# Optimization experiments

Hardware: AMD Instinct MI355X
Metric: run time of the kernel (lower is better)

Reference implementation:

```python
import jax, jax.numpy as jnp
import numpy as np

B, H0, W0, D0 = 2, 28, 28, 28
C, NH, SR, WS = 96, 6, 4, 7
N = H0 * W0 * D0
EPS = 1e-5


def _window_partition(x, ws, H, W, D):
    # x: [B, heads, N, c] -> [B*heads*nWindows, ws^3, c]
    Bn, h, Nn, c = x.shape
    x = x.reshape(Bn * h, H // ws, ws, W // ws, ws, D // ws, ws, c)
    x = x.transpose(0, 1, 3, 5, 2, 4, 6, 7)
    return x.reshape(-1, ws * ws * ws, c)


def _window_reverse(w, ws, H, W, D, heads):
    # w: [B*heads*nWindows, ws^3, c] -> [B, N, heads*c]
    c = w.shape[-1]
    nW = (H // ws) * (W // ws) * (D // ws)
    Bh = w.shape[0] // nW
    x = w.reshape(Bh, H // ws, W // ws, D // ws, ws, ws, ws, c)
    x = x.transpose(0, 1, 4, 2, 5, 3, 6, 7).reshape(Bh, H, W, D, c)
    x = x.reshape(Bh // heads, heads, H, W, D, c).transpose(0, 2, 3, 4, 1, 5)
    return x.reshape(Bh // heads, H * W * D, heads * c)


def _ln(x, g, b):
    mu = x.mean(-1, keepdims=True)
    var = ((x - mu) ** 2).mean(-1, keepdims=True)
    return (x - mu) * jax.lax.rsqrt(var + EPS) * g + b


def _forward(x, H, W, D, lepe_lin_w, lepe_lin_b, lepe_conv_w, lepe_conv_b,
             sr_w, sr_b, norm_g, norm_b, q1_w, kv1_w, q2_w, kv2_w, proj_w, proj_b):
    Bn, Nn, Cc = x.shape
    nh2 = NH // 2
    hd = Cc // NH
    scale = hd ** -0.5
    dn = ('NCDHW', 'OIDHW', 'NCDHW')
    # LePE branch: linear -> depthwise 3x3x3 conv over the 3D volume
    t = (x @ lepe_lin_w.T + lepe_lin_b).transpose(0, 2, 1).reshape(Bn, Cc, H, W, D)
    lepe = jax.lax.conv_general_dilated(t, lepe_conv_w, (1, 1, 1), [(1, 1)] * 3,
                                        dimension_numbers=dn, feature_group_count=Cc)
    lepe = (lepe + lepe_conv_b[None, :, None, None, None]).reshape(Bn, Cc, Nn).transpose(0, 2, 1)
    # Branch 1: spatial-reduction global attention on half the heads
    q1 = (x @ q1_w.T).reshape(Bn, Nn, nh2, hd).transpose(0, 2, 1, 3)  # [B,h/2,N,hd]
    x5 = x.transpose(0, 2, 1).reshape(Bn, Cc, H, W, D)
    xs = jax.lax.conv_general_dilated(x5, sr_w, (SR, SR, SR), 'VALID', dimension_numbers=dn)
    xs = (xs + sr_b[None, :, None, None, None]).reshape(Bn, Cc, -1).transpose(0, 2, 1)  # [B,Nsr,C]
    xs = jax.nn.gelu(_ln(xs, norm_g, norm_b), approximate=False)
    kv1 = (xs @ kv1_w.T).reshape(Bn, -1, 2, nh2, hd).transpose(2, 0, 3, 1, 4)
    k1, v1 = kv1[0], kv1[1]
    attn1 = jax.nn.softmax(jnp.einsum('bhnd,bhmd->bhnm', q1, k1) * scale, axis=-1)
    x1 = jnp.einsum('bhnm,bhmd->bhnd', attn1, v1).transpose(0, 2, 1, 3).reshape(Bn, Nn, Cc // 2)
    # Branch 2: 7x7x7 windowed local attention on the other half of the heads
    q2 = (x @ q2_w.T).reshape(Bn, Nn, nh2, hd).transpose(0, 2, 1, 3)
    kv2 = (x @ kv2_w.T).reshape(Bn, Nn, 2, nh2, hd).transpose(2, 0, 3, 1, 4)
    k2, v2 = kv2[0], kv2[1]
    q2w = _window_partition(q2, WS, H, W, D)
    k2w = _window_partition(k2, WS, H, W, D)
    v2w = _window_partition(v2, WS, H, W, D)
    attn2 = jax.nn.softmax(jnp.einsum('wnd,wmd->wnm', q2w, k2w) * scale, axis=-1)
    x2 = _window_reverse(jnp.einsum('wnm,wmd->wnd', attn2, v2w), WS, H, W, D, nh2)
    # Fuse branches, add LePE, project
    return (jnp.concatenate([x1, x2], axis=-1) + lepe) @ proj_w.T + proj_b


def setup_inputs() -> dict:
    key = jax.random.key(0)
    ks = jax.random.split(key, 10)
    lin = lambda k, o, i: jax.random.normal(k, (o, i), jnp.float32) * 0.02
    return {
        'x': jax.random.normal(ks[0], (B, N, C), jnp.float32),
        'H': H0, 'W': W0, 'D': D0,
        'lepe_lin_w': lin(ks[1], C, C),
        'lepe_lin_b': jnp.zeros((C,), jnp.float32),
        'lepe_conv_w': jax.random.normal(ks[2], (C, 1, 3, 3, 3), jnp.float32) * 0.27,
        'lepe_conv_b': jnp.zeros((C,), jnp.float32),
        'sr_w': jax.random.normal(ks[3], (C, C, SR, SR, SR), jnp.float32) * 0.02,
        'sr_b': jnp.zeros((C,), jnp.float32),
        'norm_g': jnp.ones((C,), jnp.float32),
        'norm_b': jnp.zeros((C,), jnp.float32),
        'q1_w': lin(ks[4], C // 2, C),
        'kv1_w': lin(ks[5], C, C),
        'q2_w': lin(ks[6], C // 2, C),
        'kv2_w': lin(ks[7], C, C),
        'proj_w': lin(ks[8], C, C),
        'proj_b': jnp.zeros((C,), jnp.float32),
    }


def reference(x, H, W, D, lepe_lin_w, lepe_lin_b, lepe_conv_w, lepe_conv_b,
              sr_w, sr_b, norm_g, norm_b, q1_w, kv1_w, q2_w, kv2_w, proj_w, proj_b):
    return _forward(x, H, W, D, lepe_lin_w, lepe_lin_b, lepe_conv_w, lepe_conv_b,
                    sr_w, sr_b, norm_g, norm_b, q1_w, kv1_w, q2_w, kv2_w, proj_w, proj_b)
```

## Files before the change

kernel.cpp:

```cpp
#include <hip/hip_runtime.h>

#define BB 2
#define NTOK 21952
#define CC 96
#define WD 784
#define NSR 343
#define NKT 22
#define NPADK 9.f
#define NSITE 686
#define SCALE 0.25f
#define LN_EPS 1e-5f
#define WSA_N (6*16*24*64)
#define WPA_N (18*6*64)

typedef _Float16 half_t;
typedef __attribute__((ext_vector_type(2))) _Float16 h2;
typedef __attribute__((ext_vector_type(4))) _Float16 h4;
typedef __attribute__((ext_vector_type(8))) _Float16 h8;
typedef __attribute__((ext_vector_type(4))) float f32x4;
union HU { h8 v; h2 p[4]; };
union H4U { h4 v; h2 p[2]; };

__device__ __forceinline__ h2 pk2(float a, float b) {
    return __builtin_bit_cast(h2, __builtin_amdgcn_cvt_pkrtz(a, b));
}

__global__ __launch_bounds__(256) void k_wt(
    const float* __restrict__ w, h4* __restrict__ WSA, h4* __restrict__ WPA,
    const float* __restrict__ lepe_w, const float* __restrict__ q1_w,
    const float* __restrict__ q2_w, const float* __restrict__ kv2_w,
    const float* __restrict__ cw, float* __restrict__ cwT)
{
    const int id = blockIdx.x * 256 + threadIdx.x;
    if (id < WSA_N) {
        const int lane = id & 63;
        const int kt = (id >> 6) % 24;
        const int ks = ((id >> 6) / 24) % 16;
        const int ct = (id >> 6) / 384;
        const int co = ct * 16 + (lane & 15);
        const int kb = ks * 384 + kt * 16 + 4 * (lane >> 4);
        const int p = kb / 96, c = kb % 96;
        float f[4];
#pragma unroll
        for (int i = 0; i < 4; i++)
            f[i] = w[(size_t)co * 6144 + (c + i) * 64 + p];
        H4U t; t.p[0] = pk2(f[0], f[1]); t.p[1] = pk2(f[2], f[3]);
        WSA[id] = t.v;
    } else if (id < WSA_N + WPA_N) {
        const int id2 = id - WSA_N;
        const int lane = id2 & 63;
        const int kt = (id2 >> 6) % 6;
        const int ct = (id2 >> 6) / 6;
        const int co = ct * 16 + (lane & 15);
        const int k = kt * 16 + 4 * (lane >> 4);
        const float* wrow;
        if (co < 96)       wrow = lepe_w + co * 96;
        else if (co < 144) wrow = q1_w + (co - 96) * 96;
        else if (co < 192) wrow = q2_w + (co - 144) * 96;
        else               wrow = kv2_w + (co - 192) * 96;
        float4 v = *(const float4*)(wrow + k);
        H4U t; t.p[0] = pk2(v.x, v.y); t.p[1] = pk2(v.z, v.w);
        WPA[id2] = t.v;
    } else if (id < WSA_N + WPA_N + 27 * 96) {
        const int id3 = id - WSA_N - WPA_N;
        const int tap = id3 / 96, c = id3 % 96;
        cwT[tap * 96 + c] = cw[c * 27 + tap];
    }
}

__global__ __launch_bounds__(256) void k_proj(
    const float* __restrict__ x, const h4* __restrict__ WPA,
    const float* __restrict__ lepe_b, float* __restrict__ P)
{
    __shared__ h4 BX[4 * 6 * 64];
    const int blk = blockIdx.x;
    const int tid = threadIdx.x;

    for (int s = tid; s < 1536; s += 256) {
        int lane = s & 63;
        int kt = (s >> 6) % 6;
        int tt = (s >> 6) / 6;
        int tok = blk * 64 + tt * 16 + (lane & 15);
        int k0 = kt * 16 + 4 * (lane >> 4);
        float4 v = *(const float4*)(x + (size_t)tok * 96 + k0);
        H4U t; t.p[0] = pk2(v.x, v.y); t.p[1] = pk2(v.z, v.w);
        BX[s] = t.v;
    }
    __syncthreads();

    const int lane = tid & 63;
    const int wid = tid >> 6;

    h4 bx[24];
#pragma unroll
    for (int q = 0; q < 24; q++) bx[q] = BX[q * 64 + lane];

    for (int ct = wid; ct < 18; ct += 4) {
        f32x4 acc[4];
#pragma unroll
        for (int tt = 0; tt < 4; tt++) acc[tt] = (f32x4){0.f, 0.f, 0.f, 0.f};
#pragma unroll
        for (int kt = 0; kt < 6; kt++) {
            h4 wa = WPA[(ct * 6 + kt) * 64 + lane];
#pragma unroll
            for (int tt = 0; tt < 4; tt++)
                acc[tt] = __builtin_amdgcn_mfma_f32_16x16x16f16(
                    wa, bx[tt * 6 + kt], acc[tt], 0, 0, 0);
        }
        float4 b4 = make_float4(0.f, 0.f, 0.f, 0.f);
        if (ct < 6) b4 = *(const float4*)(lepe_b + ct * 16 + 4 * (lane >> 4));
#pragma unroll
        for (int tt = 0; tt < 4; tt++) {
            int tok = blk * 64 + tt * 16 + (lane & 15);
            float4 o = make_float4(acc[tt][0] + b4.x, acc[tt][1] + b4.y,
                                   acc[tt][2] + b4.z, acc[tt][3] + b4.w);
            *(float4*)(P + (size_t)tok * 288 + ct * 16 + 4 * (lane >> 4)) = o;
        }
    }
}

__global__ __launch_bounds__(384) void k_sr_a(
    const float* __restrict__ x, const h4* __restrict__ WSA,
    float* __restrict__ pa)
{
    __shared__ h4 BX[24 * 64];
    const int mb = blockIdx.x;
    const int ks = blockIdx.y;
    const int tid = threadIdx.x;
    const int lane = tid & 63;
    const int ct = tid >> 6;

    for (int s = tid; s < 24 * 64; s += 384) {
        int l = s & 63;
        int kt = s >> 6;
        int site = mb * 16 + (l & 15);
        if (site > NSITE - 1) site = NSITE - 1;
        int b = site / NSR, sloc = site % NSR;
        int si = sloc / 49, sj = (sloc / 7) % 7, sk = sloc % 7;
        int kg = ks * 384 + kt * 16 + 4 * (l >> 4);
        int p = kg / 96, c = kg % 96;
        int a = p >> 4, q = (p >> 2) & 3, r = p & 3;
        int n = (4 * si + a) * WD + (4 * sj + q) * 28 + (4 * sk + r);
        float4 v = *(const float4*)(x + ((size_t)b * NTOK + n) * 96 + c);
        H4U t; t.p[0] = pk2(v.x, v.y); t.p[1] = pk2(v.z, v.w);
        BX[s] = t.v;
    }
    __syncthreads();

    const int site_g = mb * 16 + (lane & 15);
    const h4* wb = WSA + (size_t)((ct * 16 + ks) * 24) * 64 + lane;

    f32x4 acc0 = (f32x4){0.f, 0.f, 0.f, 0.f};
    f32x4 acc1 = (f32x4){0.f, 0.f, 0.f, 0.f};
#pragma unroll
    for (int kp = 0; kp < 12; kp++) {
        h4 wa0 = wb[(2 * kp) * 64];
        h4 wa1 = wb[(2 * kp + 1) * 64];
        acc0 = __builtin_amdgcn_mfma_f32_16x16x16f16(
            wa0, BX[(2 * kp) * 64 + lane], acc0, 0, 0, 0);
        acc1 = __builtin_amdgcn_mfma_f32_16x16x16f16(
            wa1, BX[(2 * kp + 1) * 64 + lane], acc1, 0, 0, 0);
    }
    if (site_g < NSITE) {
        *(float4*)(pa + ((size_t)site_g * 16 + ks) * 96 + ct * 16
                   + 4 * (lane >> 4)) =
            make_float4(acc0[0] + acc1[0], acc0[1] + acc1[1],
                        acc0[2] + acc1[2], acc0[3] + acc1[3]);
    }
}

__global__ __launch_bounds__(96) void k_sr_b(
    const float* __restrict__ pa, const float* __restrict__ sr_b,
    const float* __restrict__ norm_g, const float* __restrict__ norm_b,
    const float* __restrict__ kv1_w, float* __restrict__ k1,
    float* __restrict__ v1)
{
    __shared__ float xs_s[96];
    __shared__ float gx[96];
    const int s_g = blockIdx.x;
    const int b = s_g / NSR, s = s_g % NSR;
    const int co = threadIdx.x;

    const float* pp = pa + (size_t)s_g * 16 * 96 + co;
    float acc = sr_b[co];
#pragma unroll
    for (int ks = 0; ks < 16; ks++) acc += pp[ks * 96];
    xs_s[co] = acc;
    __syncthreads();

    float m = 0.f, m2 = 0.f;
    for (int c = 0; c < 96; c++) { float v = xs_s[c]; m += v; m2 += v * v; }
    m *= (1.f / 96.f);
    float var = m2 * (1.f / 96.f) - m * m;
    float t = (acc - m) * rsqrtf(var + LN_EPS) * norm_g[co] + norm_b[co];
    gx[co] = 0.5f * t * (1.f + erff(t * 0.70710678118654752f));
    __syncthreads();

    const float4* w4 = (const float4*)(kv1_w + co * 96);
    const float4* g4 = (const float4*)gx;
    float a2 = 0.f;
#pragma unroll
    for (int c = 0; c < 24; c++) {
        float4 w = w4[c]; float4 g = g4[c];
        a2 += g.x * w.x + g.y * w.y + g.z * w.z + g.w * w.w;
    }
    int pair = co / 48, h = (co % 48) / 16, e = co % 16;
    float* dst = pair ? v1 : k1;
    dst[(((size_t)b * 3 + h) * NSR + s) * 16 + e] = a2;
}

__device__ __forceinline__ void attn_mfma_core(
    const h4* __restrict__ KA, const h4* __restrict__ VA, int lane,
    h4 qb, f32x4& o, float& lsum)
{
    o = (f32x4){0.f, 0.f, 0.f, 0.f};
    lsum = 0.f;
    for (int t = 0; t < NKT; t++) {
        h4 ka = KA[t * 64 + lane];
        f32x4 s = __builtin_amdgcn_mfma_f32_16x16x16f16(
            ka, qb, (f32x4){0.f, 0.f, 0.f, 0.f}, 0, 0, 0);
        float p0 = __expf(s[0]), p1 = __expf(s[1]);
        float p2 = __expf(s[2]), p3 = __expf(s[3]);
        lsum += (p0 + p1) + (p2 + p3);
        H4U pb;
        pb.p[0] = pk2(p0, p1);
        pb.p[1] = pk2(p2, p3);
        h4 va = VA[t * 64 + lane];
        o = __builtin_amdgcn_mfma_f32_16x16x16f16(va, pb.v, o, 0, 0, 0);
    }
}

__global__ __launch_bounds__(512) void k_attn1(
    const float* __restrict__ P, const float* __restrict__ k1,
    const float* __restrict__ v1, float* __restrict__ y)
{
    __shared__ h4 KA[NKT * 64];
    __shared__ h4 VA[NKT * 64];
    const int bh = blockIdx.x;
    const int b = bh / 3, h = bh % 3;
    const float* ksrc = k1 + (size_t)bh * NSR * 16;
    const float* vsrc = v1 + (size_t)bh * NSR * 16;

    for (int s = threadIdx.x; s < NKT * 64; s += 512) {
        int t = s >> 6, l = s & 63;
        int key = t * 16 + (l & 15);
        int dg = (l >> 4) * 4;
        H4U tmp; tmp.p[0] = pk2(0.f, 0.f); tmp.p[1] = pk2(0.f, 0.f);
        if (key < NSR) {
            float4 v = *(const float4*)(ksrc + (size_t)key * 16 + dg);
            tmp.p[0] = pk2(v.x, v.y); tmp.p[1] = pk2(v.z, v.w);
        }
        KA[s] = tmp.v;
    }
    for (int s = threadIdx.x; s < NKT * 64; s += 512) {
        int t = s >> 6, l = s & 63;
        int dim = l & 15;
        int k0 = t * 16 + (l >> 4) * 4;
        float f[4];
#pragma unroll
        for (int i = 0; i < 4; i++) {
            int key = k0 + i;
            f[i] = (key < NSR) ? vsrc[(size_t)key * 16 + dim] : 0.f;
        }
        H4U tmp; tmp.p[0] = pk2(f[0], f[1]); tmp.p[1] = pk2(f[2], f[3]);
        VA[s] = tmp.v;
    }
    __syncthreads();

    const int lane = threadIdx.x & 63;
    const int wid = threadIdx.x >> 6;

    for (int qi = wid; qi < 16; qi += 8) {
        int qt = blockIdx.y * 16 + qi;
        if (qt >= 1372) break;
        int tok = qt * 16 + (lane & 15);
        float4 qv = *(const float4*)(P + ((size_t)b * NTOK + tok) * 288
                                     + 96 + h * 16 + (lane >> 4) * 4);
        H4U qb;
        qb.p[0] = pk2(qv.x * SCALE, qv.y * SCALE);
        qb.p[1] = pk2(qv.z * SCALE, qv.w * SCALE);

        f32x4 o; float lsum;
        attn_mfma_core(KA, VA, lane, qb.v, o, lsum);
        lsum += __shfl_xor(lsum, 16);
        lsum += __shfl_xor(lsum, 32);
        float inv = 1.f / (lsum - NPADK);
        float4 out = make_float4(o[0] * inv, o[1] * inv, o[2] * inv, o[3] * inv);
        *(float4*)(y + ((size_t)b * NTOK + tok) * 96 + h * 16 + (lane >> 4) * 4) = out;
    }
}

__global__ __launch_bounds__(512) void k_attn2(
    const float* __restrict__ P, float* __restrict__ y)
{
    __shared__ h4 KA[NKT * 64];
    __shared__ h4 VA[NKT * 64];
    const int pb = blockIdx.x;
    const int b = pb / 192;
    const int rem = pb % 192;
    const int h = rem / 64, win = rem % 64;
    const int wh = win >> 4, ww = (win >> 2) & 3, wd = win & 3;
    const int h0 = wh * 7, w0 = ww * 7, d0 = wd * 7;
    const size_t bOff = (size_t)b * NTOK;

    for (int s = threadIdx.x; s < NKT * 64; s += 512) {
        int t = s >> 6, l = s & 63;
        int key = t * 16 + (l & 15);
        int dg = (l >> 4) * 4;
        H4U tmp; tmp.p[0] = pk2(0.f, 0.f); tmp.p[1] = pk2(0.f, 0.f);
        if (key < NSR) {
            int a = key / 49, bw = (key / 7) % 7, cw = key % 7;
            int n = (h0 + a) * WD + (w0 + bw) * 28 + (d0 + cw);
            float4 v = *(const float4*)(P + (bOff + n) * 288 + 192 + h * 16 + dg);
            tmp.p[0] = pk2(v.x, v.y); tmp.p[1] = pk2(v.z, v.w);
        }
        KA[s] = tmp.v;
    }
    for (int s = threadIdx.x; s < NKT * 64; s += 512) {
        int t = s >> 6, l = s & 63;
        int dim = l & 15;
        int k0 = t * 16 + (l >> 4) * 4;
        float f[4];
#pragma unroll
        for (int i = 0; i < 4; i++) {
            int key = k0 + i;
            float val = 0.f;
            if (key < NSR) {
                int a = key / 49, bw = (key / 7) % 7, cw = key % 7;
                int n = (h0 + a) * WD + (w0 + bw) * 28 + (d0 + cw);
                val = P[(bOff + n) * 288 + 240 + h * 16 + dim];
            }
            f[i] = val;
        }
        H4U tmp; tmp.p[0] = pk2(f[0], f[1]); tmp.p[1] = pk2(f[2], f[3]);
        VA[s] = tmp.v;
    }
    __syncthreads();

    const int lane = threadIdx.x & 63;
    const int wid = threadIdx.x >> 6;

    for (int qt = wid; qt < NKT; qt += 8) {
        int q = qt * 16 + (lane & 15);
        int qc = (q < NSR) ? q : (NSR - 1);
        int ai = qc / 49, bi = (qc / 7) % 7, ci = qc % 7;
        int tok = (h0 + ai) * WD + (w0 + bi) * 28 + (d0 + ci);
        float4 qv = *(const float4*)(P + (bOff + tok) * 288
                                     + 144 + h * 16 + (lane >> 4) * 4);
        H4U qb;
        qb.p[0] = pk2(qv.x * SCALE, qv.y * SCALE);
        qb.p[1] = pk2(qv.z * SCALE, qv.w * SCALE);

        f32x4 o; float lsum;
        attn_mfma_core(KA, VA, lane, qb.v, o, lsum);
        lsum += __shfl_xor(lsum, 16);
        lsum += __shfl_xor(lsum, 32);
        float inv = 1.f / (lsum - NPADK);
        if (q < NSR) {
            float4 out = make_float4(o[0] * inv, o[1] * inv, o[2] * inv, o[3] * inv);
            *(float4*)(y + (bOff + tok) * 96 + 48 + h * 16 + (lane >> 4) * 4) = out;
        }
    }
}

__global__ __launch_bounds__(256) void k_lepe(
    const float* __restrict__ P, const float* __restrict__ cwT,
    const float* __restrict__ cb, float* __restrict__ y)
{
    const int id = blockIdx.x * 256 + threadIdx.x;
    const int g4 = (id % 24) * 4;
    const int rest = id / 24;
    const int dc = rest % 4;
    const int nw = rest / 4;
    const int w = nw % 28;
    const int h = (nw / 28) % 28;
    const int b = nw / 784;
    const int d0 = dc * 7;
    const float* Pb = P + (size_t)b * NTOK * 288;

    float4 bias = *(const float4*)(cb + g4);
    float4 acc[7];
#pragma unroll
    for (int j = 0; j < 7; j++) acc[j] = bias;

#pragma unroll
    for (int dh = -1; dh <= 1; dh++) {
#pragma unroll
        for (int dw = -1; dw <= 1; dw++) {
            const int hh = h + dh, ww = w + dw;
            const bool pok = ((unsigned)hh < 28u) & ((unsigned)ww < 28u);
            const int nbase = (pok ? hh : h) * WD + (pok ? ww : w) * 28;
            const float mp = pok ? 1.f : 0.f;
            const int tb = ((dh + 1) * 3 + (dw + 1)) * 3;
            float4 wm = *(const float4*)(cwT + (tb + 0) * 96 + g4);
            float4 w0 = *(const float4*)(cwT + (tb + 1) * 96 + g4);
            float4 wp = *(const float4*)(cwT + (tb + 2) * 96 + g4);
            wm.x *= mp; wm.y *= mp; wm.z *= mp; wm.w *= mp;
            w0.x *= mp; w0.y *= mp; w0.z *= mp; w0.w *= mp;
            wp.x *= mp; wp.y *= mp; wp.z *= mp; wp.w *= mp;

            float4 pv[9];
#pragma unroll
            for (int k = 0; k < 9; k++) {
                const int d = d0 + k - 1;
                const bool dok = (unsigned)d < 28u;
                float4 v = *(const float4*)(Pb + (size_t)(nbase + (dok ? d : 0)) * 288 + g4);
                if (!dok) v = make_float4(0.f, 0.f, 0.f, 0.f);
                pv[k] = v;
            }
#pragma unroll
            for (int j = 0; j < 7; j++) {
                acc[j].x += pv[j].x * wm.x + pv[j + 1].x * w0.x + pv[j + 2].x * wp.x;
                acc[j].y += pv[j].y * wm.y + pv[j + 1].y * w0.y + pv[j + 2].y * wp.y;
                acc[j].z += pv[j].z * wm.z + pv[j + 1].z * w0.z + pv[j + 2].z * wp.z;
                acc[j].w += pv[j].w * wm.w + pv[j + 1].w * w0.w + pv[j + 2].w * wp.w;
            }
        }
    }

    const size_t tokBase = (size_t)b * NTOK + h * WD + w * 28 + d0;
#pragma unroll
    for (int j = 0; j < 7; j++) {
        float4* yp = (float4*)(y + (tokBase + j) * 96 + g4);
        float4 cur = *yp;
        cur.x += acc[j].x; cur.y += acc[j].y;
        cur.z += acc[j].z; cur.w += acc[j].w;
        *yp = cur;
    }
}

__global__ __launch_bounds__(192) void k_out(
    const float* __restrict__ y, const float* __restrict__ proj_w,
    const float* __restrict__ proj_b, float* __restrict__ out)
{
    __shared__ h2 xh[48][68];
    __shared__ h2 wh[48][52];

    const int base = blockIdx.x * 64;
    const int j0 = blockIdx.y * 48;

    for (int it = threadIdx.x; it < 1536; it += 192) {
        int t = it & 63, cq = it >> 6;
        float4 v = *(const float4*)(y + (size_t)(base + t) * 96 + cq * 4);
        xh[cq * 2 + 0][t] = pk2(v.x, v.y);
        xh[cq * 2 + 1][t] = pk2(v.z, v.w);
    }
    for (int it = threadIdx.x; it < 1152; it += 192) {
        int jl = it % 48, cq = it / 48;
        float4 v = *(const float4*)(proj_w + (size_t)(j0 + jl) * 96 + cq * 4);
        wh[cq * 2 + 0][jl] = pk2(v.x, v.y);
        wh[cq * 2 + 1][jl] = pk2(v.z, v.w);
    }
    __syncthreads();

    const int tq = threadIdx.x & 15;
    const int jq = threadIdx.x >> 4;
    float acc[4][4];
#pragma unroll
    for (int i = 0; i < 4; i++)
#pragma unroll
        for (int jj = 0; jj < 4; jj++) acc[i][jj] = 0.f;

    for (int cp = 0; cp < 48; cp++) {
        HU xv, wv;
        xv.v = *(const h8*)(&xh[cp][tq * 4]);
        wv.v = *(const h8*)(&wh[cp][jq * 4]);
#pragma unroll
        for (int i = 0; i < 4; i++)
#pragma unroll
            for (int jj = 0; jj < 4; jj++)
                acc[i][jj] = __builtin_amdgcn_fdot2(xv.p[i], wv.p[jj], acc[i][jj], false);
    }

    float4 bias = *(const float4*)(proj_b + j0 + jq * 4);
#pragma unroll
    for (int i = 0; i < 4; i++) {
        int t = base + tq * 4 + i;
        float4 o = make_float4(acc[i][0] + bias.x, acc[i][1] + bias.y,
                               acc[i][2] + bias.z, acc[i][3] + bias.w);
        *(float4*)(out + (size_t)t * 96 + j0 + jq * 4) = o;
    }
}

extern "C" void kernel_launch(void* const* d_in, const int* in_sizes, int n_in,
                              void* d_out, int out_size, void* d_ws, size_t ws_size,
                              hipStream_t stream) {
    const float* x          = (const float*)d_in[0];
    const float* lepe_lin_w = (const float*)d_in[4];
    const float* lepe_lin_b = (const float*)d_in[5];
    const float* lepe_conv_w= (const float*)d_in[6];
    const float* lepe_conv_b= (const float*)d_in[7];
    const float* sr_w       = (const float*)d_in[8];
    const float* sr_b       = (const float*)d_in[9];
    const float* norm_g     = (const float*)d_in[10];
    const float* norm_b     = (const float*)d_in[11];
    const float* q1_w       = (const float*)d_in[12];
    const float* kv1_w      = (const float*)d_in[13];
    const float* q2_w       = (const float*)d_in[14];
    const float* kv2_w      = (const float*)d_in[15];
    const float* proj_w     = (const float*)d_in[16];
    const float* proj_b     = (const float*)d_in[17];

    float* P   = (float*)d_ws;
    float* k1  = P + (size_t)BB * NTOK * 288;
    float* v1  = k1 + (size_t)BB * 3 * NSR * 16;
    float* y   = v1 + (size_t)BB * 3 * NSR * 16;
    float* pa  = y + (size_t)BB * NTOK * 96;
    float* WSAf= pa + (size_t)NSITE * 16 * 96;
    float* WPAf= WSAf + (size_t)WSA_N * 2;
    float* cwT = WPAf + (size_t)WPA_N * 2;
    h4* WSA = (h4*)WSAf;
    h4* WPA = (h4*)WPAf;

    k_wt<<<614, 256, 0, stream>>>(sr_w, WSA, WPA, lepe_lin_w, q1_w, q2_w,
                                  kv2_w, lepe_conv_w, cwT);
    k_proj<<<686, 256, 0, stream>>>(x, WPA, lepe_lin_b, P);
    k_sr_a<<<dim3(43, 16), 384, 0, stream>>>(x, WSA, pa);
    k_sr_b<<<NSITE, 96, 0, stream>>>(pa, sr_b, norm_g, norm_b, kv1_w, k1, v1);
    k_attn1<<<dim3(6, 86), 512, 0, stream>>>(P, k1, v1, y);
    k_attn2<<<384, 512, 0, stream>>>(P, y);
    k_lepe<<<588, 256, 0, stream>>>(P, cwT, lepe_conv_b, y);
    k_out<<<dim3(686, 2), 192, 0, stream>>>(y, proj_w, proj_b, (float*)d_out);
}
```

Baseline: 218.9 us.

## Stage LePE depthwise conv input halo tile in shared memory

The depthwise 3x3x3 LePE conv kernel now loads a 6x6x30 halo tile of 8 channels into LDS per block, then each thread reads its neighbourhood from shared memory instead of issuing 81 scattered global float4 loads. This cuts the roughly nine-fold redundant global reads of the projected tensor, whose 288-float stride makes those reads poorly coalesced. In exchange it adds a block-wide sync and about 35KB of LDS per 128-thread block, which may limit occupancy. The grid doubles to 1176 smaller blocks.

```diff
diff --git a/kernel.cpp b/kernel.cpp
--- a/kernel.cpp
+++ b/kernel.cpp
@@ -363,65 +363,71 @@
     }
 }
 
-__global__ __launch_bounds__(256) void k_lepe(
+__global__ __launch_bounds__(128) void k_lepe(
     const float* __restrict__ P, const float* __restrict__ cwT,
     const float* __restrict__ cb, float* __restrict__ y)
 {
-    const int id = blockIdx.x * 256 + threadIdx.x;
-    const int g4 = (id % 24) * 4;
-    const int rest = id / 24;
-    const int dc = rest % 4;
-    const int nw = rest / 4;
-    const int w = nw % 28;
-    const int h = (nw / 28) % 28;
-    const int b = nw / 784;
-    const int d0 = dc * 7;
+    __shared__ float4 T[30 * 73];
+    const int blk = blockIdx.x;
+    const int cs = blk % 12;
+    const int hwt = (blk / 12) % 49;
+    const int b = blk / (12 * 49);
+    const int h0 = (hwt / 7) * 4, w0 = (hwt % 7) * 4;
+    const int ch0 = cs * 8;
     const float* Pb = P + (size_t)b * NTOK * 288;
 
-    float4 bias = *(const float4*)(cb + g4);
+    for (int u = threadIdx.x; u < 30 * 36 * 2; u += 128) {
+        int dd = u / 72;
+        int rem = u % 72;
+        int ih = rem / 12, iw = (rem % 12) >> 1, cg = rem & 1;
+        int hi = h0 - 1 + ih, wi = w0 - 1 + iw, di = dd - 1;
+        float4 v = make_float4(0.f, 0.f, 0.f, 0.f);
+        if (((unsigned)hi < 28u) & ((unsigned)wi < 28u) & ((unsigned)di < 28u))
+            v = *(const float4*)(Pb + (size_t)(hi * WD + wi * 28 + di) * 288
+                                 + ch0 + cg * 4);
+        T[dd * 73 + (ih * 6 + iw) * 2 + cg] = v;
+    }
+    __syncthreads();
+
+    const int cg = threadIdx.x & 1;
+    const int dr = (threadIdx.x >> 1) & 3;
+    const int hw = threadIdx.x >> 3;
+    const int hh = hw >> 2, ww = hw & 3;
+    const int d0 = dr * 7;
+    const int c4 = ch0 + cg * 4;
+
+    float4 bias = *(const float4*)(cb + c4);
     float4 acc[7];
 #pragma unroll
     for (int j = 0; j < 7; j++) acc[j] = bias;
 
 #pragma unroll
-    for (int dh = -1; dh <= 1; dh++) {
-#pragma unroll
-        for (int dw = -1; dw <= 1; dw++) {
-            const int hh = h + dh, ww = w + dw;
-            const bool pok = ((unsigned)hh < 28u) & ((unsigned)ww < 28u);
-            const int nbase = (pok ? hh : h) * WD + (pok ? ww : w) * 28;
-            const float mp = pok ? 1.f : 0.f;
-            const int tb = ((dh + 1) * 3 + (dw + 1)) * 3;
-            float4 wm = *(const float4*)(cwT + (tb + 0) * 96 + g4);
-            float4 w0 = *(const float4*)(cwT + (tb + 1) * 96 + g4);
-            float4 wp = *(const float4*)(cwT + (tb + 2) * 96 + g4);
-            wm.x *= mp; wm.y *= mp; wm.z *= mp; wm.w *= mp;
-            w0.x *= mp; w0.y *= mp; w0.z *= mp; w0.w *= mp;
-            wp.x *= mp; wp.y *= mp; wp.z *= mp; wp.w *= mp;
-
+    for (int dh = 0; dh < 3; dh++) {
+#pragma unroll
+        for (int dw = 0; dw < 3; dw++) {
+            const int tb = (dh * 3 + dw) * 3;
+            float4 wm = *(const float4*)(cwT + (tb + 0) * 96 + c4);
+            float4 w0v = *(const float4*)(cwT + (tb + 1) * 96 + c4);
+            float4 wp = *(const float4*)(cwT + (tb + 2) * 96 + c4);
+            const int base = ((hh + dh) * 6 + (ww + dw)) * 2 + cg;
             float4 pv[9];
 #pragma unroll
-            for (int k = 0; k < 9; k++) {
-                const int d = d0 + k - 1;
-                const bool dok = (unsigned)d < 28u;
-                float4 v = *(const float4*)(Pb + (size_t)(nbase + (dok ? d : 0)) * 288 + g4);
-                if (!dok) v = make_float4(0.f, 0.f, 0.f, 0.f);
-                pv[k] = v;
+            for (int k = 0; k < 9; k++)
+                pv[k] = T[(d0 + k) * 73 + base];
+#pragma unroll
+            for (int j = 0; j < 7; j++) {
+                acc[j].x += pv[j].x * wm.x + pv[j + 1].x * w0v.x + pv[j + 2].x * wp.x;
+                acc[j].y += pv[j].y * wm.y + pv[j + 1].y * w0v.y + pv[j + 2].y * wp.y;
+                acc[j].z += pv[j].z * wm.z + pv[j + 1].z * w0v.z + pv[j + 2].z * wp.z;
+                acc[j].w += pv[j].w * wm.w + pv[j + 1].w * w0v.w + pv[j + 2].w * wp.w;
             }
-#pragma unroll
-            for (int j = 0; j < 7; j++) {
-                acc[j].x += pv[j].x * wm.x + pv[j + 1].x * w0.x + pv[j + 2].x * wp.x;
-                acc[j].y += pv[j].y * wm.y + pv[j + 1].y * w0.y + pv[j + 2].y * wp.y;
-                acc[j].z += pv[j].z * wm.z + pv[j + 1].z * w0.z + pv[j + 2].z * wp.z;
-                acc[j].w += pv[j].w * wm.w + pv[j + 1].w * w0.w + pv[j + 2].w * wp.w;
-            }
-        }
-    }
-
-    const size_t tokBase = (size_t)b * NTOK + h * WD + w * 28 + d0;
+        }
+    }
+
+    const size_t tokBase = (size_t)b * NTOK + (h0 + hh) * WD + (w0 + ww) * 28 + d0;
 #pragma unroll
     for (int j = 0; j < 7; j++) {
-        float4* yp = (float4*)(y + (tokBase + j) * 96 + g4);
+        float4* yp = (float4*)(y + (tokBase + j) * 96 + c4);
         float4 cur = *yp;
         cur.x += acc[j].x; cur.y += acc[j].y;
         cur.z += acc[j].z; cur.w += acc[j].w;
@@ -519,6 +525,6 @@
     k_sr_b<<<NSITE, 96, 0, stream>>>(pa, sr_b, norm_g, norm_b, kv1_w, k1, v1);
     k_attn1<<<dim3(6, 86), 512, 0, stream>>>(P, k1, v1, y);
     k_attn2<<<384, 512, 0, stream>>>(P, y);
-    k_lepe<<<588, 256, 0, stream>>>(P, cwT, lepe_conv_b, y);
+    k_lepe<<<1176, 128, 0, stream>>>(P, cwT, lepe_conv_b, y);
     k_out<<<dim3(686, 2), 192, 0, stream>>>(y, proj_w, proj_b, (float*)d_out);
 }
```

Result: slower. 232.9 us (+6.4%).

## Store LePE linear output channel-group-major and remap depthwise conv threads

Applied to the files above, without the earlier changes.

The projection kernel now writes the LePE linear output to a separate channel-group-major buffer (one float4 per token per 4-channel group), and P keeps only the 192 q/kv channels with a narrower stride. The depthwise 3D conv kernel is reorganized so each block handles one (batch, channel group, h) row, making neighbouring-token reads contiguous float4s instead of strided 288-float rows. The aim is better coalescing and cache locality in the conv and a smaller P footprint for the attention kernels. It launches 128-thread blocks with 16 idle threads and still does read-modify-write on y with a token-major stride.

```diff
diff --git a/kernel.cpp b/kernel.cpp
--- a/kernel.cpp
+++ b/kernel.cpp
@@ -12,6 +12,7 @@
 #define LN_EPS 1e-5f
 #define WSA_N (6*16*24*64)
 #define WPA_N (18*6*64)
+#define PSTR 192
 
 typedef _Float16 half_t;
 typedef __attribute__((ext_vector_type(2))) _Float16 h2;
@@ -70,7 +71,8 @@
 
 __global__ __launch_bounds__(256) void k_proj(
     const float* __restrict__ x, const h4* __restrict__ WPA,
-    const float* __restrict__ lepe_b, float* __restrict__ P)
+    const float* __restrict__ lepe_b, float* __restrict__ P,
+    float4* __restrict__ tl)
 {
     __shared__ h4 BX[4 * 6 * 64];
     const int blk = blockIdx.x;
@@ -107,14 +109,24 @@
                 acc[tt] = __builtin_amdgcn_mfma_f32_16x16x16f16(
                     wa, bx[tt * 6 + kt], acc[tt], 0, 0, 0);
         }
-        float4 b4 = make_float4(0.f, 0.f, 0.f, 0.f);
-        if (ct < 6) b4 = *(const float4*)(lepe_b + ct * 16 + 4 * (lane >> 4));
-#pragma unroll
-        for (int tt = 0; tt < 4; tt++) {
-            int tok = blk * 64 + tt * 16 + (lane & 15);
-            float4 o = make_float4(acc[tt][0] + b4.x, acc[tt][1] + b4.y,
-                                   acc[tt][2] + b4.z, acc[tt][3] + b4.w);
-            *(float4*)(P + (size_t)tok * 288 + ct * 16 + 4 * (lane >> 4)) = o;
+        if (ct < 6) {
+            float4 b4 = *(const float4*)(lepe_b + ct * 16 + 4 * (lane >> 4));
+            const size_t cg = ct * 4 + (lane >> 4);
+#pragma unroll
+            for (int tt = 0; tt < 4; tt++) {
+                int tok = blk * 64 + tt * 16 + (lane & 15);
+                tl[cg * (BB * NTOK) + tok] =
+                    make_float4(acc[tt][0] + b4.x, acc[tt][1] + b4.y,
+                                acc[tt][2] + b4.z, acc[tt][3] + b4.w);
+            }
+        } else {
+#pragma unroll
+            for (int tt = 0; tt < 4; tt++) {
+                int tok = blk * 64 + tt * 16 + (lane & 15);
+                *(float4*)(P + (size_t)tok * PSTR + (ct - 6) * 16
+                           + 4 * (lane >> 4)) =
+                    make_float4(acc[tt][0], acc[tt][1], acc[tt][2], acc[tt][3]);
+            }
         }
     }
 }
@@ -274,8 +286,8 @@
         int qt = blockIdx.y * 16 + qi;
         if (qt >= 1372) break;
         int tok = qt * 16 + (lane & 15);
-        float4 qv = *(const float4*)(P + ((size_t)b * NTOK + tok) * 288
-                                     + 96 + h * 16 + (lane >> 4) * 4);
+        float4 qv = *(const float4*)(P + ((size_t)b * NTOK + tok) * PSTR
+                                     + h * 16 + (lane >> 4) * 4);
         H4U qb;
         qb.p[0] = pk2(qv.x * SCALE, qv.y * SCALE);
         qb.p[1] = pk2(qv.z * SCALE, qv.w * SCALE);
@@ -311,7 +323,7 @@
         if (key < NSR) {
             int a = key / 49, bw = (key / 7) % 7, cw = key % 7;
             int n = (h0 + a) * WD + (w0 + bw) * 28 + (d0 + cw);
-            float4 v = *(const float4*)(P + (bOff + n) * 288 + 192 + h * 16 + dg);
+            float4 v = *(const float4*)(P + (bOff + n) * PSTR + 96 + h * 16 + dg);
             tmp.p[0] = pk2(v.x, v.y); tmp.p[1] = pk2(v.z, v.w);
         }
         KA[s] = tmp.v;
@@ -328,7 +340,7 @@
             if (key < NSR) {
                 int a = key / 49, bw = (key / 7) % 7, cw = key % 7;
                 int n = (h0 + a) * WD + (w0 + bw) * 28 + (d0 + cw);
-                val = P[(bOff + n) * 288 + 240 + h * 16 + dim];
+                val = P[(bOff + n) * PSTR + 144 + h * 16 + dim];
             }
             f[i] = val;
         }
@@ -345,8 +357,8 @@
         int qc = (q < NSR) ? q : (NSR - 1);
         int ai = qc / 49, bi = (qc / 7) % 7, ci = qc % 7;
         int tok = (h0 + ai) * WD + (w0 + bi) * 28 + (d0 + ci);
-        float4 qv = *(const float4*)(P + (bOff + tok) * 288
-                                     + 144 + h * 16 + (lane >> 4) * 4);
+        float4 qv = *(const float4*)(P + (bOff + tok) * PSTR
+                                     + 48 + h * 16 + (lane >> 4) * 4);
         H4U qb;
         qb.p[0] = pk2(qv.x * SCALE, qv.y * SCALE);
         qb.p[1] = pk2(qv.z * SCALE, qv.w * SCALE);
@@ -363,57 +375,62 @@
     }
 }
 
-__global__ __launch_bounds__(256) void k_lepe(
-    const float* __restrict__ P, const float* __restrict__ cwT,
+__global__ __launch_bounds__(128) void k_lepe(
+    const float4* __restrict__ tl, const float* __restrict__ cwT,
     const float* __restrict__ cb, float* __restrict__ y)
 {
-    const int id = blockIdx.x * 256 + threadIdx.x;
-    const int g4 = (id % 24) * 4;
-    const int rest = id / 24;
-    const int dc = rest % 4;
-    const int nw = rest / 4;
-    const int w = nw % 28;
-    const int h = (nw / 28) % 28;
-    const int b = nw / 784;
-    const int d0 = dc * 7;
-    const float* Pb = P + (size_t)b * NTOK * 288;
-
-    float4 bias = *(const float4*)(cb + g4);
+    const int blk = blockIdx.x;
+    const int h = blk % 28;
+    const int cg = (blk / 28) % 24;
+    const int b = blk / (28 * 24);
+    const int t = threadIdx.x;
+    if (t >= 112) return;
+    const int w = t >> 2;
+    const int dq = t & 3;
+    const int d0 = dq * 7;
+    const int c4 = cg * 4;
+
+    const float4* base = tl + (size_t)cg * (BB * NTOK) + (size_t)b * NTOK;
+
+    float4 bias = *(const float4*)(cb + c4);
     float4 acc[7];
 #pragma unroll
     for (int j = 0; j < 7; j++) acc[j] = bias;
 
 #pragma unroll
     for (int dh = -1; dh <= 1; dh++) {
+        const int hh = h + dh;
+        const bool hok = (unsigned)hh < 28u;
 #pragma unroll
         for (int dw = -1; dw <= 1; dw++) {
-            const int hh = h + dh, ww = w + dw;
-            const bool pok = ((unsigned)hh < 28u) & ((unsigned)ww < 28u);
-            const int nbase = (pok ? hh : h) * WD + (pok ? ww : w) * 28;
+            const int ww = w + dw;
+            const bool pok = hok & ((unsigned)ww < 28u);
             const float mp = pok ? 1.f : 0.f;
             const int tb = ((dh + 1) * 3 + (dw + 1)) * 3;
-            float4 wm = *(const float4*)(cwT + (tb + 0) * 96 + g4);
-            float4 w0 = *(const float4*)(cwT + (tb + 1) * 96 + g4);
-            float4 wp = *(const float4*)(cwT + (tb + 2) * 96 + g4);
+            float4 wm = *(const float4*)(cwT + (tb + 0) * 96 + c4);
+            float4 w0v = *(const float4*)(cwT + (tb + 1) * 96 + c4);
+            float4 wp = *(const float4*)(cwT + (tb + 2) * 96 + c4);
             wm.x *= mp; wm.y *= mp; wm.z *= mp; wm.w *= mp;
-            w0.x *= mp; w0.y *= mp; w0.z *= mp; w0.w *= mp;
+            w0v.x *= mp; w0v.y *= mp; w0v.z *= mp; w0v.w *= mp;
             wp.x *= mp; wp.y *= mp; wp.z *= mp; wp.w *= mp;
 
+            const float4* pp = base + (pok ? (hh * WD + ww * 28)
+                                           : (h * WD + w * 28));
             float4 pv[9];
 #pragma unroll
             for (int k = 0; k < 9; k++) {
-                const int d = d0 + k - 1;
+                const int d = d0 - 1 + k;
                 const bool dok = (unsigned)d < 28u;
-                float4 v = *(const float4*)(Pb + (size_t)(nbase + (dok ? d : 0)) * 288 + g4);
+                float4 v = pp[dok ? d : 0];
                 if (!dok) v = make_float4(0.f, 0.f, 0.f, 0.f);
                 pv[k] = v;
             }
 #pragma unroll
             for (int j = 0; j < 7; j++) {
-                acc[j].x += pv[j].x * wm.x + pv[j + 1].x * w0.x + pv[j + 2].x * wp.x;
-                acc[j].y += pv[j].y * wm.y + pv[j + 1].y * w0.y + pv[j + 2].y * wp.y;
-                acc[j].z += pv[j].z * wm.z + pv[j + 1].z * w0.z + pv[j + 2].z * wp.z;
-                acc[j].w += pv[j].w * wm.w + pv[j + 1].w * w0.w + pv[j + 2].w * wp.w;
+                acc[j].x += pv[j].x * wm.x + pv[j + 1].x * w0v.x + pv[j + 2].x * wp.x;
+                acc[j].y += pv[j].y * wm.y + pv[j + 1].y * w0v.y + pv[j + 2].y * wp.y;
+                acc[j].z += pv[j].z * wm.z + pv[j + 1].z * w0v.z + pv[j + 2].z * wp.z;
+                acc[j].w += pv[j].w * wm.w + pv[j + 1].w * w0v.w + pv[j + 2].w * wp.w;
             }
         }
     }
@@ -421,7 +438,7 @@
     const size_t tokBase = (size_t)b * NTOK + h * WD + w * 28 + d0;
 #pragma unroll
     for (int j = 0; j < 7; j++) {
-        float4* yp = (float4*)(y + (tokBase + j) * 96 + g4);
+        float4* yp = (float4*)(y + (tokBase + j) * 96 + c4);
         float4 cur = *yp;
         cur.x += acc[j].x; cur.y += acc[j].y;
         cur.z += acc[j].z; cur.w += acc[j].w;
@@ -502,7 +519,8 @@
     const float* proj_b     = (const float*)d_in[17];
 
     float* P   = (float*)d_ws;
-    float* k1  = P + (size_t)BB * NTOK * 288;
+    float* tlf = P + (size_t)BB * NTOK * PSTR;
+    float* k1  = tlf + (size_t)24 * BB * NTOK * 4;
     float* v1  = k1 + (size_t)BB * 3 * NSR * 16;
     float* y   = v1 + (size_t)BB * 3 * NSR * 16;
     float* pa  = y + (size_t)BB * NTOK * 96;
@@ -511,14 +529,15 @@
     float* cwT = WPAf + (size_t)WPA_N * 2;
     h4* WSA = (h4*)WSAf;
     h4* WPA = (h4*)WPAf;
+    float4* tl = (float4*)tlf;
 
     k_wt<<<614, 256, 0, stream>>>(sr_w, WSA, WPA, lepe_lin_w, q1_w, q2_w,
                                   kv2_w, lepe_conv_w, cwT);
-    k_proj<<<686, 256, 0, stream>>>(x, WPA, lepe_lin_b, P);
+    k_proj<<<686, 256, 0, stream>>>(x, WPA, lepe_lin_b, P, tl);
     k_sr_a<<<dim3(43, 16), 384, 0, stream>>>(x, WSA, pa);
     k_sr_b<<<NSITE, 96, 0, stream>>>(pa, sr_b, norm_g, norm_b, kv1_w, k1, v1);
     k_attn1<<<dim3(6, 86), 512, 0, stream>>>(P, k1, v1, y);
     k_attn2<<<384, 512, 0, stream>>>(P, y);
-    k_lepe<<<588, 256, 0, stream>>>(P, cwT, lepe_conv_b, y);
+    k_lepe<<<1344, 128, 0, stream>>>(tl, cwT, lepe_conv_b, y);
     k_out<<<dim3(686, 2), 192, 0, stream>>>(y, proj_w, proj_b, (float*)d_out);
 }
```

Result: no change. 219.6 us (+0.3%).
